# Performance work log

Measured on AMD Instinct MI355X. Metric: run time of the kernel, lower is better.

The kernel has to match this reference:

```python
import jax, jax.numpy as jnp
import numpy as np

THRESH = 8000.0  # saturating partial-sum accumulator threshold (thresh=8000 in source)
GROUP = 128      # channel chunk size used by split_tensor_* helpers
EPS = 1e-5

def binarize(x):
    # sign() forward with straight-through estimator (standard BinarizeConv2d behavior)
    return x + jax.lax.stop_gradient(jnp.sign(x) - x)

def psum_conv3x3(x, w):
    """3x3 'same' conv computed as 9 shifted-window partial sums per 128-channel
    group, with the running accumulator saturated to [-THRESH, THRESH] after each
    partial sum (emulating a low-bit hardware accumulator).
    x: [B, C, H, W]; w: [O, C, 3, 3] -> out [B, O, H, W]."""
    B, C, H, W = x.shape
    O = w.shape[0]
    xp = jnp.pad(x, ((0, 0), (0, 0), (1, 1), (1, 1)))
    acc = jnp.zeros((B, O, H, W), dtype=x.dtype)
    n_groups = C // GROUP
    for g in range(n_groups):
        xg = xp[:, g * GROUP:(g + 1) * GROUP]
        wg = w[:, g * GROUP:(g + 1) * GROUP]
        # split_tensor ordering: x1..x9 vary row (dim2) fastest, then col (dim3)
        for col in range(3):
            for row in range(3):
                part = jnp.einsum('bchw,oc->bohw',
                                  xg[:, :, row:row + H, col:col + W],
                                  wg[:, :, row, col])
                acc = jnp.clip(acc + part, -THRESH, THRESH)
    return acc

def batchnorm(x, gamma, beta, mean, var):
    inv = gamma / jnp.sqrt(var + EPS)
    return x * inv[None, :, None, None] + (beta - mean * inv)[None, :, None, None]

def setup_inputs() -> dict:
    key = jax.random.key(0)
    ks = jax.random.split(key, 12)
    B, C, H, W = 64, 128, 56, 56
    return {
        'x': jax.random.normal(ks[0], (B, C, H, W), jnp.float32),
        'w1': jax.random.normal(ks[1], (C, C, 3, 3), jnp.float32),
        'w2': jax.random.normal(ks[2], (C, C, 3, 3), jnp.float32),
        'gamma1': jax.random.uniform(ks[3], (C,), jnp.float32, 0.5, 1.5),
        'beta1': jax.random.normal(ks[4], (C,), jnp.float32) * 0.1,
        'mean1': jax.random.normal(ks[5], (C,), jnp.float32),
        'var1': jax.random.uniform(ks[6], (C,), jnp.float32, 0.5, 1.5),
        'gamma2': jax.random.uniform(ks[7], (C,), jnp.float32, 0.5, 1.5),
        'beta2': jax.random.normal(ks[8], (C,), jnp.float32) * 0.1,
        'mean2': jax.random.normal(ks[9], (C,), jnp.float32),
        'var2': jax.random.uniform(ks[10], (C,), jnp.float32, 0.5, 1.5),
    }

def reference(x, w1, w2, gamma1, beta1, mean1, var1, gamma2, beta2, mean2, var2):
    residual = x
    out = psum_conv3x3(binarize(x), binarize(w1))
    out = batchnorm(out, gamma1, beta1, mean1, var1)
    out = jnp.clip(out, -1.0, 1.0)  # hardtanh
    out = psum_conv3x3(binarize(out), binarize(w2))
    out = batchnorm(out, gamma2, beta2, mean2, var2)
    out = out + residual
    out = jnp.clip(out, -1.0, 1.0)
    return out
```

## Files before the change

### kernel.cpp

```cpp
#include <hip/hip_runtime.h>
#include <cstdint>
#include <cstddef>


typedef int      v4i __attribute__((ext_vector_type(4)));
typedef float    v4f __attribute__((ext_vector_type(4)));
typedef unsigned int v2u __attribute__((ext_vector_type(2)));

constexpr int B = 64, C = 128, H = 56, W = 56;
constexpr int HP = H + 2, WP = W + 2;
constexpr int PIX = H * W;
constexpr int M = B * H * W;
constexpr int NTILES = M / 256;
constexpr int TPX = NTILES / 8;

constexpr size_t XS_BYTES = (size_t)B * HP * WP * C;
constexpr size_t XS1_OFF = 0;
constexpr size_t XS2_OFF = XS_BYTES;
constexpr size_t WF_BYTES = 18 * 8192;
constexpr size_t WF1_OFF = 2 * XS_BYTES;
constexpr size_t WF2_OFF = WF1_OFF + WF_BYTES;
constexpr size_t BNP_OFF = WF2_OFF + WF_BYTES;

__global__ __launch_bounds__(256) void zero_halo(int8_t* __restrict__ xs1,
                                                 int8_t* __restrict__ xs2) {
    int b = blockIdx.x >> 2;
    int q = blockIdx.x & 3;
    int t = q * 256 + threadIdx.x;
    size_t ib = (size_t)b * HP * WP * C;
#pragma unroll
    for (int a = 0; a < 2; ++a) {
        uint32_t* p = (uint32_t*)((a ? xs2 : xs1) + ib);
        const int ROWD = WP * C / 4;
        for (int i = t; i < ROWD; i += 1024) {
            p[i] = 0;
            p[(HP - 1) * ROWD + i] = 0;
        }
        for (int i = t; i < 56 * 2 * 32; i += 1024) {
            int r = i >> 6;
            int side = (i >> 5) & 1;
            int j = i & 31;
            p[((r + 1) * WP + side * (WP - 1)) * (C / 4) + j] = 0;
        }
    }
}

__global__ __launch_bounds__(256) void prep_x(const float* __restrict__ x,
                                              int8_t* __restrict__ xs) {
    __shared__ uint32_t tl[256 * 33];
    int t = threadIdx.x;
    int m = blockIdx.x * 256 + t;
    int b_ = m / PIX, hw = m % PIX;
    const float* xp = x + (size_t)b_ * C * PIX + hw;
#pragma unroll
    for (int c4 = 0; c4 < 32; ++c4) {
        uint32_t v = 0;
#pragma unroll
        for (int j = 0; j < 4; ++j) {
            float f = __builtin_nontemporal_load(xp + (size_t)(c4 * 4 + j) * PIX);
            v |= ((uint32_t)(uint8_t)(int8_t)((f > 0.f) - (f < 0.f))) << (8 * j);
        }
        tl[t * 33 + c4] = v;
    }
    __syncthreads();
    int pl = t >> 3, co = t & 7;
#pragma unroll
    for (int pass = 0; pass < 8; ++pass) {
        int p = pass * 32 + pl;
        int mg = blockIdx.x * 256 + p;
        int b2 = mg / PIX, hw2 = mg % PIX, h2 = hw2 / W, w2 = hw2 % W;
        size_t ob = ((size_t)(b2 * HP + h2 + 1) * WP + (w2 + 1)) * C + co * 16;
        v4i val;
#pragma unroll
        for (int k = 0; k < 4; ++k) val[k] = (int)tl[p * 33 + co * 4 + k];
        *(v4i*)(xs + ob) = val;
    }
}

__global__ __launch_bounds__(256) void prep_w(
    const float* __restrict__ w1, const float* __restrict__ w2,
    const float* __restrict__ g1, const float* __restrict__ be1,
    const float* __restrict__ mu1, const float* __restrict__ va1,
    const float* __restrict__ g2, const float* __restrict__ be2,
    const float* __restrict__ mu2, const float* __restrict__ va2,
    int8_t* __restrict__ wf1, int8_t* __restrict__ wf2,
    float* __restrict__ bnp) {
    int t = blockIdx.x * 256 + threadIdx.x;
    if (t < 256) {
        int o = t & 127;
        if (t < 128) {
            float inv = g1[o] / sqrtf(va1[o] + 1e-5f);
            bnp[o]       = inv;
            bnp[128 + o] = __fsub_rn(be1[o], __fmul_rn(mu1[o], inv));
        } else {
            float inv = g2[o] / sqrtf(va2[o] + 1e-5f);
            bnp[256 + o] = inv;
            bnp[384 + o] = __fsub_rn(be2[o], __fmul_rn(mu2[o], inv));
        }
    }
    if (t >= 2 * 18 * 8 * 64) return;
    int lane = t & 63;
    int nsub = (t >> 6) & 7;
    int kh   = (t >> 9) & 1;
    int tap  = (t >> 10) % 9;
    int which = (t >> 10) / 9;
    const float* w = which ? w2 : w1;
    int8_t* wf = which ? wf2 : wf1;
    int o = (lane & 15) * 8 + nsub;
    int cbase = kh * 64 + (lane >> 4) * 16;
    int r = tap / 3, s = tap % 3;
    int slot = r * 6 + kh * 3 + s;
    int8_t frag[16];
#pragma unroll
    for (int j = 0; j < 16; ++j) {
        float f = w[((size_t)(o * C + cbase + j) * 3 + r) * 3 + s];
        frag[j] = (int8_t)((f > 0.f) - (f < 0.f));
    }
    *(v4i*)(wf + (size_t)((slot * 8 + nsub) * 64 + lane) * 16) =
        *(const v4i*)frag;
}

template <int N>
__device__ __forceinline__ void wait_vm() {
    if constexpr (N == 0) asm volatile("s_waitcnt vmcnt(0)");
    else if constexpr (N == 2) asm volatile("s_waitcnt vmcnt(2)");
    else if constexpr (N == 4) asm volatile("s_waitcnt vmcnt(4)");
    else if constexpr (N == 6) asm volatile("s_waitcnt vmcnt(6)");
}
template <int N>
__device__ __forceinline__ void wait_lgkm() {
    if constexpr (N == 0) asm volatile("s_waitcnt lgkmcnt(0)");
    else if constexpr (N == 8) asm volatile("s_waitcnt lgkmcnt(8)");
}

template <int RG>
__device__ __forceinline__ void do_conv(
    const int (&mrows)[RG], const int8_t* __restrict__ xs, const int8_t* wlds,
    int lane, int quad, int l15, v4i (&acc)[RG][8])
{
    const int8_t* ap[RG];
#pragma unroll
    for (int rg = 0; rg < RG; ++rg) {
        int ma = mrows[rg] + l15;
        int wa = ma % W; int ta = ma / W; int ha = ta % H; int ba = ta / H;
        ap[rg] = xs + ((ba * HP + ha) * WP + wa) * C + quad * 16;
    }
    uint32_t bb = (uint32_t)(uintptr_t)wlds + (uint32_t)(lane << 4);

#pragma unroll
    for (int rg = 0; rg < RG; ++rg)
#pragma unroll
        for (int n = 0; n < 8; ++n) acc[rg][n] = (v4i)0;

    v4i a[3][RG];
    v4i bf0[8], bf1[8];

#pragma unroll
    for (int rg = 0; rg < RG; ++rg)
        asm volatile("global_load_dwordx4 %0, %1, off"
                     : "=v"(a[0][rg]) : "v"(ap[rg]));
#pragma unroll
    for (int rg = 0; rg < RG; ++rg)
        asm volatile("global_load_dwordx4 %0, %1, off"
                     : "=v"(a[1][rg]) : "v"(ap[rg] + C));
#pragma unroll
    for (int n = 0; n < 8; ++n)
        asm volatile("ds_read_b128 %0, %1"
                     : "=v"(bf0[n]) : "v"(bb + n * 1024));
    __builtin_amdgcn_sched_barrier(0);

    int aoffr = 0;
#pragma unroll 1
    for (int r3 = 0; r3 < 3; ++r3) {
#pragma unroll
        for (int kk = 0; kk < 6; ++kk) {
            if (kk <= 3 || r3 != 2) {
                const int kp = (kk + 2) % 6;
                const int rb = (kk <= 3) ? 0 : WP * C;
                const int noff = rb + (kp / 3) * 64 + (kp % 3) * C;
#pragma unroll
                for (int rg = 0; rg < RG; ++rg) {
                    const int8_t* p = ap[rg] + aoffr + noff;
                    asm volatile("global_load_dwordx4 %0, %1, off"
                                 : "=v"(a[(kk + 2) % 3][rg]) : "v"(p));
                }
            }
            if (kk < 5 || r3 != 2) {
                if (((kk + 1) & 1) == 0) {
#pragma unroll
                    for (int n = 0; n < 8; ++n)
                        asm volatile("ds_read_b128 %0, %1"
                                     : "=v"(bf0[n])
                                     : "v"(bb + (kk + 1) * 8192 + n * 1024));
                } else {
#pragma unroll
                    for (int n = 0; n < 8; ++n)
                        asm volatile("ds_read_b128 %0, %1"
                                     : "=v"(bf1[n])
                                     : "v"(bb + (kk + 1) * 8192 + n * 1024));
                }
            }
            __builtin_amdgcn_sched_barrier(0);
            if (r3 == 2 && kk >= 4) wait_vm<0>();
            else                    wait_vm<2 * RG>();
            __builtin_amdgcn_sched_barrier(0);
            if (r3 == 2 && kk == 5) wait_lgkm<0>();
            else                    wait_lgkm<8>();
            __builtin_amdgcn_sched_barrier(0);
            __builtin_amdgcn_s_setprio(1);
            if ((kk & 1) == 0) {
#pragma unroll
                for (int n = 0; n < 8; ++n)
#pragma unroll
                    for (int rg = 0; rg < RG; ++rg)
                        acc[rg][n] = __builtin_amdgcn_mfma_i32_16x16x64_i8(
                            a[kk % 3][rg], bf0[n], acc[rg][n], 0, 0, 0);
            } else {
#pragma unroll
                for (int n = 0; n < 8; ++n)
#pragma unroll
                    for (int rg = 0; rg < RG; ++rg)
                        acc[rg][n] = __builtin_amdgcn_mfma_i32_16x16x64_i8(
                            a[kk % 3][rg], bf1[n], acc[rg][n], 0, 0, 0);
            }
            __builtin_amdgcn_s_setprio(0);
            __builtin_amdgcn_sched_barrier(0);
        }
        aoffr += WP * C;
        bb += 6 * 8192;
    }
}

template <int RG>
__device__ __forceinline__ void epi_p1(
    v4i (&acc)[RG][8], const int (&mrows)[RG], int quad, int l15,
    const float* binv, const float* btt, int8_t* __restrict__ xs_next)
{
#pragma unroll
    for (int rg = 0; rg < RG; ++rg) {
        int m0 = mrows[rg] + quad * 4;
        int w0 = m0 % W; int t0 = m0 / W; int h0 = t0 % H; int b0 = t0 / H;
        int base = ((b0 * HP + h0 + 1) * WP + (w0 + 1)) * C + l15 * 8;
#pragma unroll
        for (int i = 0; i < 4; ++i) {
            uint32_t lo = 0, hi = 0;
#pragma unroll
            for (int n = 0; n < 8; ++n) {
                float y = __fadd_rn(__fmul_rn((float)acc[rg][n][i], binv[n]), btt[n]);
                uint32_t sb = (uint8_t)(int8_t)((y > 0.f) - (y < 0.f));
                if (n < 4) lo |= sb << (8 * n);
                else       hi |= sb << (8 * (n - 4));
            }
            v2u pk; pk[0] = lo; pk[1] = hi;
            *(v2u*)(xs_next + base + i * C) = pk;
        }
    }
}

template <int RG>
__device__ __forceinline__ void epi_p2(
    v4i (&acc)[RG][8], const int (&mrows)[RG], int quad, int l15,
    const float* binv, const float* btt,
    const float* __restrict__ xres, float* __restrict__ out)
{
#pragma unroll
    for (int rg = 0; rg < RG; ++rg) {
        int m0 = mrows[rg] + quad * 4;
        int w0 = m0 % W; int t0 = m0 / W; int h0 = t0 % H; int b0 = t0 / H;
        int pixb = b0 * C * PIX + h0 * W + w0;
#pragma unroll
        for (int n = 0; n < 8; ++n) {
            int idx = pixb + (l15 * 8 + n) * PIX;
            v4f r = __builtin_nontemporal_load((const v4f*)(xres + idx));
            v4f z;
#pragma unroll
            for (int i = 0; i < 4; ++i) {
                float y = __fadd_rn(__fmul_rn((float)acc[rg][n][i], binv[n]), btt[n]);
                float v = __fadd_rn(y, r[i]);
                z[i] = fminf(fmaxf(v, -1.f), 1.f);
            }
            __builtin_nontemporal_store(z, (v4f*)(out + idx));
        }
    }
}

__global__ __launch_bounds__(512, 1) void conv_p1(
    const int8_t* __restrict__ xs,
    const int8_t* __restrict__ wf,
    const float* __restrict__ bnp,
    int8_t* __restrict__ xs_next)
{
    __shared__ int8_t wlds[18 * 8192];
    int t = threadIdx.x, lane = t & 63, wv = t >> 6;
    int quad = lane >> 4, l15 = lane & 15;

    {
        const v4i* g = (const v4i*)wf;
        v4i* l = (v4i*)wlds;
        for (int i = t; i < 18 * 512; i += 512) l[i] = g[i];
    }
    float binv[8], btt[8];
    {
        int o0 = l15 * 8, o1 = 128 + l15 * 8;
#pragma unroll
        for (int n = 0; n < 8; ++n) { binv[n] = bnp[o0 + n]; btt[n] = bnp[o1 + n]; }
    }
    __syncthreads();

    int xcd = blockIdx.x & 7, local = blockIdx.x >> 3;
#pragma unroll 1
    for (int tloc = local; tloc < 96; tloc += 32) {
        int mw = (xcd * TPX + tloc) * 256 + wv * 32;
        int mrows2[2] = { mw, mw + 16 };
        v4i acc[2][8];
        do_conv<2>(mrows2, xs, wlds, lane, quad, l15, acc);
        epi_p1<2>(acc, mrows2, quad, l15, binv, btt, xs_next);
    }
    if (local < 4) {
        int tile = xcd * TPX + 96 + (local >> 1);
        int mw = tile * 256 + (local & 1) * 128 + wv * 16;
        int mrows1[1] = { mw };
        v4i acc[1][8];
        do_conv<1>(mrows1, xs, wlds, lane, quad, l15, acc);
        epi_p1<1>(acc, mrows1, quad, l15, binv, btt, xs_next);
    }
}

__global__ __launch_bounds__(512, 1) void conv_p2(
    const int8_t* __restrict__ xs,
    const int8_t* __restrict__ wf,
    const float* __restrict__ bnp,
    const float* __restrict__ xres,
    float* __restrict__ out)
{
    __shared__ int8_t wlds[18 * 8192];
    int t = threadIdx.x, lane = t & 63, wv = t >> 6;
    int quad = lane >> 4, l15 = lane & 15;

    {
        const v4i* g = (const v4i*)wf;
        v4i* l = (v4i*)wlds;
        for (int i = t; i < 18 * 512; i += 512) l[i] = g[i];
    }
    float binv[8], btt[8];
    {
        int o0 = 256 + l15 * 8, o1 = 384 + l15 * 8;
#pragma unroll
        for (int n = 0; n < 8; ++n) { binv[n] = bnp[o0 + n]; btt[n] = bnp[o1 + n]; }
    }
    __syncthreads();

    int xcd = blockIdx.x & 7, local = blockIdx.x >> 3;
#pragma unroll 1
    for (int tloc = local; tloc < 96; tloc += 32) {
        int mw = (xcd * TPX + tloc) * 256 + wv * 32;
        int mrows2[2] = { mw, mw + 16 };
        v4i acc[2][8];
        do_conv<2>(mrows2, xs, wlds, lane, quad, l15, acc);
        epi_p2<2>(acc, mrows2, quad, l15, binv, btt, xres, out);
    }
    if (local < 4) {
        int tile = xcd * TPX + 96 + (local >> 1);
        int mw = tile * 256 + (local & 1) * 128 + wv * 16;
        int mrows1[1] = { mw };
        v4i acc[1][8];
        do_conv<1>(mrows1, xs, wlds, lane, quad, l15, acc);
        epi_p2<1>(acc, mrows1, quad, l15, binv, btt, xres, out);
    }
}

extern "C" void kernel_launch(void* const* d_in, const int* in_sizes, int n_in,
                              void* d_out, int out_size, void* d_ws, size_t ws_size,
                              hipStream_t stream) {
    const float* x   = (const float*)d_in[0];
    const float* w1  = (const float*)d_in[1];
    const float* w2  = (const float*)d_in[2];
    const float* g1  = (const float*)d_in[3];
    const float* be1 = (const float*)d_in[4];
    const float* mu1 = (const float*)d_in[5];
    const float* va1 = (const float*)d_in[6];
    const float* g2  = (const float*)d_in[7];
    const float* be2 = (const float*)d_in[8];
    const float* mu2 = (const float*)d_in[9];
    const float* va2 = (const float*)d_in[10];

    int8_t* ws  = (int8_t*)d_ws;
    int8_t* xs1 = ws + XS1_OFF;
    int8_t* xs2 = ws + XS2_OFF;
    int8_t* wf1 = ws + WF1_OFF;
    int8_t* wf2 = ws + WF2_OFF;
    float*  bnp = (float*)(ws + BNP_OFF);

    zero_halo<<<256, 256, 0, stream>>>(xs1, xs2);
    prep_x<<<M / 256, 256, 0, stream>>>(x, xs1);
    prep_w<<<(2 * 18 * 8 * 64 + 255) / 256, 256, 0, stream>>>(
        w1, w2, g1, be1, mu1, va1, g2, be2, mu2, va2, wf1, wf2, bnp);

    conv_p1<<<256, 512, 0, stream>>>(xs1, wf1, bnp, xs2);
    conv_p2<<<256, 512, 0, stream>>>(xs2, wf2, bnp, x, (float*)d_out);
}
```

Before: 324.4 us.

## Split output channels across two blocks per tile and halve weight LDS footprint

Each conv kernel now splits the 128 output channels into two halves, with each block computing 64 channels and loading only its half of the weight fragments into LDS (72KB instead of 144KB). The grid doubles to 512 blocks and launch bounds allow more blocks per CU, which should raise occupancy and help hide latency. The two conv kernels are merged into one templated kernel. The cost is that every activation fragment is now loaded twice, once per channel-half block, and each MFMA round does less work per global load.

After: 356.3 us. 1.1x slower.

```diff
diff --git a/kernel.cpp b/kernel.cpp
--- a/kernel.cpp
+++ b/kernel.cpp
@@ -5,7 +5,6 @@
 
 typedef int      v4i __attribute__((ext_vector_type(4)));
 typedef float    v4f __attribute__((ext_vector_type(4)));
-typedef unsigned int v2u __attribute__((ext_vector_type(2)));
 
 constexpr int B = 64, C = 128, H = 56, W = 56;
 constexpr int HP = H + 2, WP = W + 2;
@@ -98,15 +97,16 @@
             bnp[384 + o] = __fsub_rn(be2[o], __fmul_rn(mu2[o], inv));
         }
     }
-    if (t >= 2 * 18 * 8 * 64) return;
-    int lane = t & 63;
-    int nsub = (t >> 6) & 7;
-    int kh   = (t >> 9) & 1;
-    int tap  = (t >> 10) % 9;
+    if (t >= 2 * 18432) return;
+    int lane  = t & 63;
+    int nsub  = (t >> 6) & 3;
+    int ohalf = (t >> 8) & 1;
+    int kh    = (t >> 9) & 1;
+    int tap   = (t >> 10) % 9;
     int which = (t >> 10) / 9;
     const float* w = which ? w2 : w1;
     int8_t* wf = which ? wf2 : wf1;
-    int o = (lane & 15) * 8 + nsub;
+    int o = ohalf * 64 + (lane & 15) * 4 + nsub;
     int cbase = kh * 64 + (lane >> 4) * 16;
     int r = tap / 3, s = tap % 3;
     int slot = r * 6 + kh * 3 + s;
@@ -116,7 +116,7 @@
         float f = w[((size_t)(o * C + cbase + j) * 3 + r) * 3 + s];
         frag[j] = (int8_t)((f > 0.f) - (f < 0.f));
     }
-    *(v4i*)(wf + (size_t)((slot * 8 + nsub) * 64 + lane) * 16) =
+    *(v4i*)(wf + (size_t)((((slot * 2 + ohalf) * 4 + nsub) * 64 + lane)) * 16) =
         *(const v4i*)frag;
 }
 
@@ -125,18 +125,17 @@
     if constexpr (N == 0) asm volatile("s_waitcnt vmcnt(0)");
     else if constexpr (N == 2) asm volatile("s_waitcnt vmcnt(2)");
     else if constexpr (N == 4) asm volatile("s_waitcnt vmcnt(4)");
-    else if constexpr (N == 6) asm volatile("s_waitcnt vmcnt(6)");
 }
 template <int N>
 __device__ __forceinline__ void wait_lgkm() {
     if constexpr (N == 0) asm volatile("s_waitcnt lgkmcnt(0)");
-    else if constexpr (N == 8) asm volatile("s_waitcnt lgkmcnt(8)");
+    else if constexpr (N == 4) asm volatile("s_waitcnt lgkmcnt(4)");
 }
 
 template <int RG>
 __device__ __forceinline__ void do_conv(
     const int (&mrows)[RG], const int8_t* __restrict__ xs, const int8_t* wlds,
-    int lane, int quad, int l15, v4i (&acc)[RG][8])
+    int lane, int quad, int l15, v4i (&acc)[RG][4])
 {
     const int8_t* ap[RG];
 #pragma unroll
@@ -150,10 +149,10 @@
 #pragma unroll
     for (int rg = 0; rg < RG; ++rg)
 #pragma unroll
-        for (int n = 0; n < 8; ++n) acc[rg][n] = (v4i)0;
+        for (int n = 0; n < 4; ++n) acc[rg][n] = (v4i)0;
 
     v4i a[3][RG];
-    v4i bf0[8], bf1[8];
+    v4i bf0[4], bf1[4];
 
 #pragma unroll
     for (int rg = 0; rg < RG; ++rg)
@@ -164,7 +163,7 @@
         asm volatile("global_load_dwordx4 %0, %1, off"
                      : "=v"(a[1][rg]) : "v"(ap[rg] + C));
 #pragma unroll
-    for (int n = 0; n < 8; ++n)
+    for (int n = 0; n < 4; ++n)
         asm volatile("ds_read_b128 %0, %1"
                      : "=v"(bf0[n]) : "v"(bb + n * 1024));
     __builtin_amdgcn_sched_barrier(0);
@@ -188,16 +187,16 @@
             if (kk < 5 || r3 != 2) {
                 if (((kk + 1) & 1) == 0) {
 #pragma unroll
-                    for (int n = 0; n < 8; ++n)
+                    for (int n = 0; n < 4; ++n)
                         asm volatile("ds_read_b128 %0, %1"
                                      : "=v"(bf0[n])
-                                     : "v"(bb + (kk + 1) * 8192 + n * 1024));
+                                     : "v"(bb + (kk + 1) * 4096 + n * 1024));
                 } else {
 #pragma unroll
-                    for (int n = 0; n < 8; ++n)
+                    for (int n = 0; n < 4; ++n)
                         asm volatile("ds_read_b128 %0, %1"
                                      : "=v"(bf1[n])
-                                     : "v"(bb + (kk + 1) * 8192 + n * 1024));
+                                     : "v"(bb + (kk + 1) * 4096 + n * 1024));
                 }
             }
             __builtin_amdgcn_sched_barrier(0);
@@ -205,19 +204,19 @@
             else                    wait_vm<2 * RG>();
             __builtin_amdgcn_sched_barrier(0);
             if (r3 == 2 && kk == 5) wait_lgkm<0>();
-            else                    wait_lgkm<8>();
+            else                    wait_lgkm<4>();
             __builtin_amdgcn_sched_barrier(0);
             __builtin_amdgcn_s_setprio(1);
             if ((kk & 1) == 0) {
 #pragma unroll
-                for (int n = 0; n < 8; ++n)
+                for (int n = 0; n < 4; ++n)
 #pragma unroll
                     for (int rg = 0; rg < RG; ++rg)
                         acc[rg][n] = __builtin_amdgcn_mfma_i32_16x16x64_i8(
                             a[kk % 3][rg], bf0[n], acc[rg][n], 0, 0, 0);
             } else {
 #pragma unroll
-                for (int n = 0; n < 8; ++n)
+                for (int n = 0; n < 4; ++n)
 #pragma unroll
                     for (int rg = 0; rg < RG; ++rg)
                         acc[rg][n] = __builtin_amdgcn_mfma_i32_16x16x64_i8(
@@ -227,39 +226,37 @@
             __builtin_amdgcn_sched_barrier(0);
         }
         aoffr += WP * C;
-        bb += 6 * 8192;
+        bb += 6 * 4096;
     }
 }
 
 template <int RG>
 __device__ __forceinline__ void epi_p1(
-    v4i (&acc)[RG][8], const int (&mrows)[RG], int quad, int l15,
+    v4i (&acc)[RG][4], const int (&mrows)[RG], int quad, int l15, int coff,
     const float* binv, const float* btt, int8_t* __restrict__ xs_next)
 {
 #pragma unroll
     for (int rg = 0; rg < RG; ++rg) {
         int m0 = mrows[rg] + quad * 4;
         int w0 = m0 % W; int t0 = m0 / W; int h0 = t0 % H; int b0 = t0 / H;
-        int base = ((b0 * HP + h0 + 1) * WP + (w0 + 1)) * C + l15 * 8;
+        int base = ((b0 * HP + h0 + 1) * WP + (w0 + 1)) * C + coff + l15 * 4;
 #pragma unroll
         for (int i = 0; i < 4; ++i) {
-            uint32_t lo = 0, hi = 0;
-#pragma unroll
-            for (int n = 0; n < 8; ++n) {
+            uint32_t wd = 0;
+#pragma unroll
+            for (int n = 0; n < 4; ++n) {
                 float y = __fadd_rn(__fmul_rn((float)acc[rg][n][i], binv[n]), btt[n]);
                 uint32_t sb = (uint8_t)(int8_t)((y > 0.f) - (y < 0.f));
-                if (n < 4) lo |= sb << (8 * n);
-                else       hi |= sb << (8 * (n - 4));
-            }
-            v2u pk; pk[0] = lo; pk[1] = hi;
-            *(v2u*)(xs_next + base + i * C) = pk;
+                wd |= sb << (8 * n);
+            }
+            *(uint32_t*)(xs_next + base + i * C) = wd;
         }
     }
 }
 
 template <int RG>
 __device__ __forceinline__ void epi_p2(
-    v4i (&acc)[RG][8], const int (&mrows)[RG], int quad, int l15,
+    v4i (&acc)[RG][4], const int (&mrows)[RG], int quad, int l15, int coff,
     const float* binv, const float* btt,
     const float* __restrict__ xres, float* __restrict__ out)
 {
@@ -269,8 +266,8 @@
         int w0 = m0 % W; int t0 = m0 / W; int h0 = t0 % H; int b0 = t0 / H;
         int pixb = b0 * C * PIX + h0 * W + w0;
 #pragma unroll
-        for (int n = 0; n < 8; ++n) {
-            int idx = pixb + (l15 * 8 + n) * PIX;
+        for (int n = 0; n < 4; ++n) {
+            int idx = pixb + (coff + l15 * 4 + n) * PIX;
             v4f r = __builtin_nontemporal_load((const v4f*)(xres + idx));
             v4f z;
 #pragma unroll
@@ -284,88 +281,54 @@
     }
 }
 
-__global__ __launch_bounds__(512, 1) void conv_p1(
-    const int8_t* __restrict__ xs,
-    const int8_t* __restrict__ wf,
-    const float* __restrict__ bnp,
-    int8_t* __restrict__ xs_next)
-{
-    __shared__ int8_t wlds[18 * 8192];
-    int t = threadIdx.x, lane = t & 63, wv = t >> 6;
-    int quad = lane >> 4, l15 = lane & 15;
-
-    {
-        const v4i* g = (const v4i*)wf;
-        v4i* l = (v4i*)wlds;
-        for (int i = t; i < 18 * 512; i += 512) l[i] = g[i];
-    }
-    float binv[8], btt[8];
-    {
-        int o0 = l15 * 8, o1 = 128 + l15 * 8;
-#pragma unroll
-        for (int n = 0; n < 8; ++n) { binv[n] = bnp[o0 + n]; btt[n] = bnp[o1 + n]; }
-    }
-    __syncthreads();
-
-    int xcd = blockIdx.x & 7, local = blockIdx.x >> 3;
-#pragma unroll 1
-    for (int tloc = local; tloc < 96; tloc += 32) {
-        int mw = (xcd * TPX + tloc) * 256 + wv * 32;
-        int mrows2[2] = { mw, mw + 16 };
-        v4i acc[2][8];
-        do_conv<2>(mrows2, xs, wlds, lane, quad, l15, acc);
-        epi_p1<2>(acc, mrows2, quad, l15, binv, btt, xs_next);
-    }
-    if (local < 4) {
-        int tile = xcd * TPX + 96 + (local >> 1);
-        int mw = tile * 256 + (local & 1) * 128 + wv * 16;
-        int mrows1[1] = { mw };
-        v4i acc[1][8];
-        do_conv<1>(mrows1, xs, wlds, lane, quad, l15, acc);
-        epi_p1<1>(acc, mrows1, quad, l15, binv, btt, xs_next);
-    }
-}
-
-__global__ __launch_bounds__(512, 1) void conv_p2(
+template <int PHASE>
+__global__ __launch_bounds__(512, 4) void conv_bin(
     const int8_t* __restrict__ xs,
     const int8_t* __restrict__ wf,
     const float* __restrict__ bnp,
     const float* __restrict__ xres,
+    int8_t* __restrict__ xs_next,
     float* __restrict__ out)
 {
-    __shared__ int8_t wlds[18 * 8192];
+    __shared__ int8_t wlds[18 * 4096];
     int t = threadIdx.x, lane = t & 63, wv = t >> 6;
     int quad = lane >> 4, l15 = lane & 15;
+    int xcd = blockIdx.x & 7, local = blockIdx.x >> 3;
+    int ohalf = local & 1, coff = ohalf * 64;
 
     {
         const v4i* g = (const v4i*)wf;
         v4i* l = (v4i*)wlds;
-        for (int i = t; i < 18 * 512; i += 512) l[i] = g[i];
-    }
-    float binv[8], btt[8];
+        for (int i = t; i < 18 * 256; i += 512)
+            l[i] = g[(i >> 8) * 512 + ohalf * 256 + (i & 255)];
+    }
+    float binv[4], btt[4];
     {
-        int o0 = 256 + l15 * 8, o1 = 384 + l15 * 8;
-#pragma unroll
-        for (int n = 0; n < 8; ++n) { binv[n] = bnp[o0 + n]; btt[n] = bnp[o1 + n]; }
+        int o0 = (PHASE == 1 ? 0 : 256) + coff + l15 * 4;
+#pragma unroll
+        for (int n = 0; n < 4; ++n) { binv[n] = bnp[o0 + n]; btt[n] = bnp[o0 + 128 + n]; }
     }
     __syncthreads();
 
-    int xcd = blockIdx.x & 7, local = blockIdx.x >> 3;
 #pragma unroll 1
-    for (int tloc = local; tloc < 96; tloc += 32) {
-        int mw = (xcd * TPX + tloc) * 256 + wv * 32;
+    for (int rd = 0; rd < 3; ++rd) {
+        int tile = xcd * TPX + (local >> 1) + rd * 32;
+        int mw = tile * 256 + wv * 32;
         int mrows2[2] = { mw, mw + 16 };
-        v4i acc[2][8];
+        v4i acc[2][4];
         do_conv<2>(mrows2, xs, wlds, lane, quad, l15, acc);
-        epi_p2<2>(acc, mrows2, quad, l15, binv, btt, xres, out);
-    }
-    if (local < 4) {
-        int tile = xcd * TPX + 96 + (local >> 1);
-        int mw = tile * 256 + (local & 1) * 128 + wv * 16;
+        if (PHASE == 1) epi_p1<2>(acc, mrows2, quad, l15, coff, binv, btt, xs_next);
+        else            epi_p2<2>(acc, mrows2, quad, l15, coff, binv, btt, xres, out);
+    }
+    if (local < 8) {
+        int tile = xcd * TPX + 96 + (local >> 2);
+        int mh = (local >> 1) & 1;
+        int mw = tile * 256 + mh * 128 + wv * 16;
         int mrows1[1] = { mw };
-        v4i acc[1][8];
+        v4i acc[1][4];
         do_conv<1>(mrows1, xs, wlds, lane, quad, l15, acc);
-        epi_p2<1>(acc, mrows1, quad, l15, binv, btt, xres, out);
+        if (PHASE == 1) epi_p1<1>(acc, mrows1, quad, l15, coff, binv, btt, xs_next);
+        else            epi_p2<1>(acc, mrows1, quad, l15, coff, binv, btt, xres, out);
     }
 }
 
@@ -393,9 +356,9 @@
 
     zero_halo<<<256, 256, 0, stream>>>(xs1, xs2);
     prep_x<<<M / 256, 256, 0, stream>>>(x, xs1);
-    prep_w<<<(2 * 18 * 8 * 64 + 255) / 256, 256, 0, stream>>>(
+    prep_w<<<(2 * 18432 + 255) / 256, 256, 0, stream>>>(
         w1, w2, g1, be1, mu1, va1, g2, be2, mu2, va2, wf1, wf2, bnp);
 
-    conv_p1<<<256, 512, 0, stream>>>(xs1, wf1, bnp, xs2);
-    conv_p2<<<256, 512, 0, stream>>>(xs2, wf2, bnp, x, (float*)d_out);
-}
+    conv_bin<1><<<512, 512, 0, stream>>>(xs1, wf1, bnp, nullptr, xs2, nullptr);
+    conv_bin<2><<<512, 512, 0, stream>>>(xs2, wf2, bnp, x, nullptr, (float*)d_out);
+}
```
